# Performance work log

Hardware: AMD Instinct MI355X
Metric: run time of the kernel (lower is better)

## Reference

```python
import jax, jax.numpy as jnp
import numpy as np

N, E, B = 65536, 524288, 256
FEAT, EMB, NH, NB, NC = 64, 128, 4, 2, 4
OUT = EMB // NH
SLOPE = 0.01  # LeakyReLU negative_slope used everywhere in the module


def lrelu(x):
    return jnp.where(x > 0, x, SLOPE * x)


def seg_softmax(logits, seg, nseg, mask):
    # PyG softmax(src, batch): exp(x - segment_max) / (segment_sum + 1e-16)
    z = jnp.where(mask, logits, -jnp.inf)
    m = jax.ops.segment_max(z, seg, num_segments=nseg)
    m = jnp.where(jnp.isfinite(m), m, 0.0)
    e = jnp.exp(z - m[seg])
    s = jax.ops.segment_sum(e, seg, num_segments=nseg)
    return e / (s[seg] + 1e-16)


def topk_pool(x, seg, w, min_score, nseg):
    # PyG TopKPooling with min_score: score = softmax(x.w, batch);
    # keep nodes with score > min(min_score, per-graph max - 1e-7); x_out = x*score.
    score = x @ w  # [N]
    sm = seg_softmax(score, seg, nseg, jnp.ones(score.shape, bool))
    smax = jax.ops.segment_max(sm, seg, num_segments=nseg)
    thr = jnp.minimum(smax - 1e-7, min_score)
    keep = sm > thr[seg]
    xp = jnp.where(keep[:, None], x * sm[:, None], 0.0)
    return xp, keep


def graph_conv_max(x, src, dst, emask, Wrel, Wroot, b, n):
    # PyG GraphConv(aggr='max'): out = Wrel @ max_{j in N(i)} x_j + Wroot @ x_i + b
    msg = jnp.where(emask[:, None], x[src], -jnp.inf)  # [E, d]
    agg = jax.ops.segment_max(msg, dst, num_segments=n)
    agg = jnp.where(jnp.isfinite(agg), agg, 0.0)  # nodes with no in-edges -> 0 (PyG scatter fill)
    return agg @ Wrel.T + x @ Wroot.T + b


def batchnorm(x, g, b):
    # training-mode BatchNorm1d: batch statistics, biased variance, eps=1e-5
    mu = x.mean(0)
    var = x.var(0)
    return g * (x - mu) * jax.lax.rsqrt(var + 1e-5) + b


def setup_inputs() -> dict:
    key = jax.random.key(0)
    ks = jax.random.split(key, 16)
    s_feat = np.float32(1.0 / np.sqrt(FEAT))
    s_emb = np.float32(1.0 / np.sqrt(EMB))
    return {
        "x": jax.random.normal(ks[0], (N, FEAT), jnp.float32),
        "edge_index": jax.random.randint(ks[1], (2, E), 0, N, jnp.int32),
        "batch": (jnp.arange(N, dtype=jnp.int32) // (N // B)).astype(jnp.int32),
        "W_rel0": jax.random.normal(ks[2], (EMB, FEAT), jnp.float32) * s_feat,
        "W_root0": jax.random.normal(ks[3], (EMB, FEAT), jnp.float32) * s_feat,
        "b0": jnp.zeros((EMB,), jnp.float32),
        "bn0_g": jnp.ones((EMB,), jnp.float32),
        "bn0_b": jnp.zeros((EMB,), jnp.float32),
        "blk_pool_w": jax.random.normal(ks[4], (NB, NH, EMB), jnp.float32) * s_emb,
        "blk_Wrel": jax.random.normal(ks[5], (NB, NH, OUT, EMB), jnp.float32) * s_emb,
        "blk_Wroot": jax.random.normal(ks[6], (NB, NH, OUT, EMB), jnp.float32) * s_emb,
        "blk_b": jnp.zeros((NB, NH, OUT), jnp.float32),
        "blk_bn_g": jnp.ones((NB, EMB), jnp.float32),
        "blk_bn_b": jnp.zeros((NB, EMB), jnp.float32),
        "cls_pool_w": jax.random.normal(ks[7], (NC, EMB), jnp.float32) * s_emb,
        "cls_gW1": jax.random.normal(ks[8], (NC, EMB, EMB), jnp.float32) * s_emb,
        "cls_gb1": jnp.zeros((NC, EMB), jnp.float32),
        "cls_gW2": jax.random.normal(ks[9], (NC, EMB), jnp.float32) * s_emb,
        "cls_gb2": jnp.zeros((NC,), jnp.float32),
        "cls_fW1": jax.random.normal(ks[10], (NC, EMB, EMB), jnp.float32) * s_emb,
        "cls_fb1": jnp.zeros((NC, EMB), jnp.float32),
        "cls_fW2": jax.random.normal(ks[11], (NC, EMB), jnp.float32) * s_emb,
        "cls_fb2": jnp.zeros((NC,), jnp.float32),
        "batch_size": B,
    }


def reference(x, edge_index, batch, W_rel0, W_root0, b0, bn0_g, bn0_b,
              blk_pool_w, blk_Wrel, blk_Wroot, blk_b, blk_bn_g, blk_bn_b,
              cls_pool_w, cls_gW1, cls_gb1, cls_gW2, cls_gb2,
              cls_fW1, cls_fb1, cls_fW2, cls_fb2, batch_size):
    n = x.shape[0]
    src, dst = edge_index[0], edge_index[1]
    all_e = jnp.ones(src.shape, bool)
    # conv0 -> leaky_relu -> bn0
    h = lrelu(graph_conv_max(x, src, dst, all_e, W_rel0, W_root0, b0, n))
    cur = batchnorm(h, bn0_g, bn0_b)
    # multi-head blocks: pool (min_score=0.7) -> GraphConv(max) per head, scatter
    # back to original node slots, concat heads, bn, residual 0.5*(x + 0.5*bn(new))
    for bi in range(NB):
        heads = []
        for hi in range(NH):
            xp, keep = topk_pool(cur, batch, blk_pool_w[bi, hi], 0.7, batch_size)
            emask = keep[src] & keep[dst]
            o = lrelu(graph_conv_max(xp, src, dst, emask,
                                     blk_Wrel[bi, hi], blk_Wroot[bi, hi],
                                     blk_b[bi, hi], n))
            heads.append(jnp.where(keep[:, None], o, 0.0))
        new = batchnorm(jnp.concatenate(heads, axis=-1), blk_bn_g[bi], blk_bn_b[bi])
        cur = 0.5 * (cur + 0.5 * new)
    # classification heads: pool (min_score=0.8) -> GlobalAttention -> MLP -> 1
    outs = []
    for c in range(NC):
        xp, keep = topk_pool(cur, batch, cls_pool_w[c], 0.8, batch_size)
        gate = lrelu(xp @ cls_gW1[c].T + cls_gb1[c]) @ cls_gW2[c] + cls_gb2[c]  # [N]
        a = seg_softmax(gate, batch, batch_size, keep)
        pooled = jax.ops.segment_sum(a[:, None] * xp, batch, num_segments=batch_size)  # [B, EMB]
        y = lrelu(pooled @ cls_fW1[c].T + cls_fb1[c]) @ cls_fW2[c] + cls_fb2[c]  # [B]
        outs.append(y)
    logits = jnp.stack(outs, axis=-1)  # [B, NC]
    return jax.nn.log_softmax(logits, axis=-1)
```

## Files before the change

kernel.cpp:

```cpp
#include <hip/hip_runtime.h>
#include <math.h>

#define NN 65536
#define NE 524288
#define NG 256
#define SLOPE 0.01f

__device__ __forceinline__ float lrelu(float v){ return v > 0.f ? v : SLOPE*v; }

__device__ __forceinline__ float blockMax4(float v, float* s4){
  #pragma unroll
  for(int o=32;o>0;o>>=1) v = fmaxf(v, __shfl_down(v, o, 64));
  int t = threadIdx.x;
  __syncthreads();
  if((t&63)==0) s4[t>>6] = v;
  __syncthreads();
  return fmaxf(fmaxf(s4[0], s4[1]), fmaxf(s4[2], s4[3]));
}
__device__ __forceinline__ float blockSum4(float v, float* s4){
  #pragma unroll
  for(int o=32;o>0;o>>=1) v += __shfl_down(v, o, 64);
  int t = threadIdx.x;
  __syncthreads();
  if((t&63)==0) s4[t>>6] = v;
  __syncthreads();
  return (s4[0]+s4[1])+(s4[2]+s4[3]);
}

__global__ __launch_bounds__(256) void k_count(const int* __restrict__ ei, int* __restrict__ deg){
  int e = blockIdx.x*256 + threadIdx.x;
  if(e < NE) atomicAdd(&deg[ei[NE + e]], 1);
}

__global__ __launch_bounds__(1024) void k_scan(const int* __restrict__ deg,
      int* __restrict__ offs, int* __restrict__ cursor){
  __shared__ int part[1024];
  int t = threadIdx.x;
  const int4* d4 = (const int4*)(deg + t*64);
  int4 buf[16];
  int s=0;
  #pragma unroll
  for(int i=0;i<16;i++){ buf[i]=d4[i]; s += buf[i].x+buf[i].y+buf[i].z+buf[i].w; }
  part[t]=s;
  __syncthreads();
  for(int off=1; off<1024; off<<=1){
    int v = (t>=off)? part[t-off] : 0;
    __syncthreads();
    part[t] += v;
    __syncthreads();
  }
  int run = (t==0)? 0 : part[t-1];
  #pragma unroll
  for(int i=0;i<16;i++){
    int4 d = buf[i];
    int4 o;
    o.x = run; run += d.x;
    o.y = run; run += d.y;
    o.z = run; run += d.z;
    o.w = run; run += d.w;
    ((int4*)(offs + t*64))[i] = o;
    ((int4*)(cursor + t*64))[i] = o;
  }
  if(t==1023) offs[NN] = run;
}

__global__ __launch_bounds__(256) void k_scatter(const int* __restrict__ ei,
      int* __restrict__ cursor, int* __restrict__ csr){
  int e = blockIdx.x*256 + threadIdx.x;
  if(e < NE){
    int d = ei[NE + e];
    int p = atomicAdd(&cursor[d], 1);
    csr[p] = ei[e];
  }
}

__global__ __launch_bounds__(256) void k_agg0(const float* __restrict__ x,
    const int* __restrict__ offs, const int* __restrict__ csr, float* __restrict__ agg0){
  int tid = blockIdx.x*256 + threadIdx.x;
  int node = tid>>4, q = tid&15;
  int e0 = offs[node], e1 = offs[node+1];
  float4 acc = make_float4(0.f,0.f,0.f,0.f);
  if(e0 < e1){
    acc = make_float4(-INFINITY,-INFINITY,-INFINITY,-INFINITY);
    int e = e0;
    for(; e+7 < e1; e += 8){
      int si[8];
      #pragma unroll
      for(int u=0;u<8;u++) si[u] = csr[e+u];
      float4 v[8];
      #pragma unroll
      for(int u=0;u<8;u++) v[u] = ((const float4*)x)[si[u]*16 + q];
      #pragma unroll
      for(int u=0;u<8;u++){
        acc.x=fmaxf(acc.x,v[u].x); acc.y=fmaxf(acc.y,v[u].y);
        acc.z=fmaxf(acc.z,v[u].z); acc.w=fmaxf(acc.w,v[u].w);
      }
    }
    for(; e < e1; e++){
      int s0 = csr[e];
      float4 v0 = ((const float4*)x)[s0*16 + q];
      acc.x=fmaxf(acc.x,v0.x); acc.y=fmaxf(acc.y,v0.y);
      acc.z=fmaxf(acc.z,v0.z); acc.w=fmaxf(acc.w,v0.w);
    }
  }
  ((float4*)agg0)[node*16 + q] = acc;
}

__global__ __launch_bounds__(256)
__attribute__((amdgpu_waves_per_eu(1,2)))
void k_conv0mm(
    const float* __restrict__ agg0, const float* __restrict__ x,
    const float* __restrict__ Wrel, const float* __restrict__ Wroot,
    const float* __restrict__ b0, float* __restrict__ cur,
    float* __restrict__ bnsum, float* __restrict__ bnsq){
  __shared__ float4 As[2048];
  __shared__ float4 Ws[2048];
  const int t = threadIdx.x;
  const int tn = t & 15;
  const int tc = t >> 4;
  float acc[8][8];
  #pragma unroll
  for(int i=0;i<8;i++)
    #pragma unroll
    for(int j=0;j<8;j++) acc[i][j]=0.f;

  const size_t tileoff = (size_t)blockIdx.x * 8192;
  #pragma unroll 1
  for(int ch=0; ch<2; ch++){
    const float4* gA = (const float4*)((ch==0? agg0 : x) + tileoff);
    const float4* gW = (const float4*)(ch==0? Wrel : Wroot);
    __syncthreads();
    #pragma unroll
    for(int i=0;i<8;i++){
      int idx = t + i*256;
      int n = idx>>4, k4 = idx&15;
      int sw = n*16 + ((k4 + (n>>3))&15);
      As[sw] = gA[idx];
      Ws[sw] = gW[idx];
    }
    __syncthreads();
    #pragma unroll 4
    for(int k4=0;k4<16;k4++){
      float4 a4[8], w4[8];
      #pragma unroll
      for(int i=0;i<8;i++) a4[i] = As[(tn*8+i)*16 + ((k4+tn)&15)];
      #pragma unroll
      for(int i=0;i<8;i++) w4[i] = Ws[(tc*8+i)*16 + ((k4+tc)&15)];
      #pragma unroll
      for(int i=0;i<8;i++)
        #pragma unroll
        for(int j=0;j<8;j++){
          acc[i][j] = fmaf(a4[i].x, w4[j].x, acc[i][j]);
          acc[i][j] = fmaf(a4[i].y, w4[j].y, acc[i][j]);
          acc[i][j] = fmaf(a4[i].z, w4[j].z, acc[i][j]);
          acc[i][j] = fmaf(a4[i].w, w4[j].w, acc[i][j]);
        }
    }
  }

  float bj[8];
  #pragma unroll
  for(int j=0;j<8;j++) bj[j] = b0[tc*8+j];
  float cs[8], cq[8];
  #pragma unroll
  for(int j=0;j<8;j++){ cs[j]=0.f; cq[j]=0.f; }
  const int nbase = blockIdx.x*128;
  #pragma unroll
  for(int i=0;i<8;i++){
    int node = nbase + tn*8 + i;
    float v[8];
    #pragma unroll
    for(int j=0;j<8;j++){
      v[j] = lrelu(acc[i][j] + bj[j]);
      cs[j] += v[j]; cq[j] += v[j]*v[j];
    }
    float4 o0 = make_float4(v[0],v[1],v[2],v[3]);
    float4 o1 = make_float4(v[4],v[5],v[6],v[7]);
    ((float4*)cur)[node*32 + tc*2 + 0] = o0;
    ((float4*)cur)[node*32 + tc*2 + 1] = o1;
  }
  __syncthreads();
  float* reds = (float*)As;
  float* redq = (float*)Ws;
  #pragma unroll
  for(int j=0;j<8;j++){
    reds[(tc*8+j)*16 + tn] = cs[j];
    redq[(tc*8+j)*16 + tn] = cq[j];
  }
  __syncthreads();
  if(t<128){
    float S=0.f, Q=0.f;
    #pragma unroll
    for(int i=0;i<16;i++){ S += reds[t*16+i]; Q += redq[t*16+i]; }
    atomicAdd(&bnsum[t], S);
    atomicAdd(&bnsq[t], Q);
  }
}

template<int MODE>
__global__ __launch_bounds__(256) void k_stream(
    float* __restrict__ cur, const float* __restrict__ onew,
    const unsigned char* __restrict__ keepin,
    const float* __restrict__ bnsA, const float* __restrict__ bnqA,
    const float* __restrict__ g1, const float* __restrict__ b1,
    const float* __restrict__ bns0, const float* __restrict__ bnq0,
    const float* __restrict__ g0, const float* __restrict__ b0bn,
    const float* __restrict__ pw, float* __restrict__ scores){
  __shared__ __align__(16) float w[4][128];
  __shared__ __align__(16) float sc1[128], of1[128], sc0[128], of0[128];
  const int t = threadIdx.x;
  if(t<128){
    if(MODE>=1){
      float mu = bnsA[t]*(1.0f/NN);
      float var = bnqA[t]*(1.0f/NN) - mu*mu;
      float s = g1[t]*rsqrtf(var+1e-5f);
      sc1[t]=s; of1[t]=b1[t]-mu*s;
    }
    if(MODE<=1){
      float mu0 = bns0[t]*(1.0f/NN);
      float var0 = bnq0[t]*(1.0f/NN) - mu0*mu0;
      float s0 = g0[t]*rsqrtf(var0+1e-5f);
      sc0[t]=s0; of0[t]=b0bn[t]-mu0*s0;
    }
  }
  __syncthreads();
  for(int i=t;i<512;i+=256){
    float wv = pw[i];
    if(MODE==0) wv *= sc0[i&127];
    w[i>>7][i&127]=wv;
  }
  __syncthreads();
  const int tid = blockIdx.x*256 + t;
  const int n = tid>>5, k = tid&31;
  float4 v = ((const float4*)cur)[tid];
  if(MODE>=1){
    const int h = k>>3;
    float4 nv = make_float4(0.f,0.f,0.f,0.f);
    if((keepin[n]>>h)&1) nv = ((const float4*)onew)[tid];
    float4 s1 = *(const float4*)&sc1[k*4];
    float4 o1 = *(const float4*)&of1[k*4];
    if(MODE==1){
      float4 s0 = *(const float4*)&sc0[k*4];
      float4 o0 = *(const float4*)&of0[k*4];
      v.x = 0.5f*(s0.x*v.x+o0.x) + 0.25f*(s1.x*nv.x+o1.x);
      v.y = 0.5f*(s0.y*v.y+o0.y) + 0.25f*(s1.y*nv.y+o1.y);
      v.z = 0.5f*(s0.z*v.z+o0.z) + 0.25f*(s1.z*nv.z+o1.z);
      v.w = 0.5f*(s0.w*v.w+o0.w) + 0.25f*(s1.w*nv.w+o1.w);
    } else {
      v.x = 0.5f*v.x + 0.25f*(s1.x*nv.x+o1.x);
      v.y = 0.5f*v.y + 0.25f*(s1.y*nv.y+o1.y);
      v.z = 0.5f*v.z + 0.25f*(s1.z*nv.z+o1.z);
      v.w = 0.5f*v.w + 0.25f*(s1.w*nv.w+o1.w);
    }
    ((float4*)cur)[tid] = v;
  }
  float sch[4];
  #pragma unroll
  for(int h2=0;h2<4;h2++){
    float4 wv = *(const float4*)&w[h2][k*4];
    sch[h2] = v.x*wv.x + v.y*wv.y + v.z*wv.z + v.w*wv.w;
  }
  #pragma unroll
  for(int o=16;o>0;o>>=1){
    #pragma unroll
    for(int h2=0;h2<4;h2++) sch[h2] += __shfl_down(sch[h2], o, 32);
  }
  if(k==0) ((float4*)scores)[n] = make_float4(sch[0],sch[1],sch[2],sch[3]);
}

__global__ __launch_bounds__(256) void k_poolsel(const float* __restrict__ scores,
    float minscore, float* __restrict__ sm4, unsigned char* __restrict__ keep,
    int* __restrict__ cnt, int* __restrict__ wl){
  __shared__ float red[4];
  const int t = threadIdx.x, g = blockIdx.x, n = g*256 + t;
  float4 s4 = ((const float4*)scores)[n];
  float scv[4] = {s4.x, s4.y, s4.z, s4.w};
  float4 smout;
  unsigned kb = 0;
  #pragma unroll 1
  for(int h=0;h<4;h++){
    float m = blockMax4(scv[h], red);
    float e = expf(scv[h]-m);
    float ssum = blockSum4(e, red);
    float sm = e/(ssum + 1e-16f);
    float smax = blockMax4(sm, red);
    float thr = fminf(smax - 1e-7f, minscore);
    ((float*)&smout)[h] = sm;
    if(sm > thr){
      kb |= (1u<<h);
      int p = atomicAdd(cnt, 1);
      wl[p] = (h<<16) | n;
    }
  }
  __syncthreads();
  ((float4*)sm4)[n] = smout;
  keep[n] = (unsigned char)kb;
}

__global__ __launch_bounds__(256) void k_blockconv(const float* __restrict__ cur,
    const int* __restrict__ offs, const int* __restrict__ csr,
    const unsigned char* __restrict__ keep, const float* __restrict__ sm4,
    const int* __restrict__ cnt, const int* __restrict__ wl,
    const float* __restrict__ Wrel, const float* __restrict__ Wroot,
    const float* __restrict__ bias,
    float* __restrict__ onew, float* __restrict__ bnsum, float* __restrict__ bnsq,
    const float* __restrict__ bns0, const float* __restrict__ bnq0,
    const float* __restrict__ g0, const float* __restrict__ b0bn, int fold){
  __shared__ __align__(16) float aggs[8][128];
  __shared__ __align__(16) float xps[8][128];
  __shared__ __align__(16) float scv[128];
  __shared__ __align__(16) float ofv[128];
  const int t = threadIdx.x, grp = t>>5, lane = t&31;
  if(t<128){
    float sv = 1.f, ov = 0.f;
    if(fold){
      float mu = bns0[t]*(1.0f/NN);
      float var = bnq0[t]*(1.0f/NN) - mu*mu;
      sv = g0[t]*rsqrtf(var+1e-5f);
      ov = b0bn[t] - mu*sv;
    }
    scv[t]=sv; ofv[t]=ov;
  }
  __syncthreads();
  const float4 s4l = *(const float4*)&scv[lane*4];
  const float4 o4l = *(const float4*)&ofv[lane*4];
  const int total = *cnt;
  for(int item = blockIdx.x*8 + grp; item < total; item += gridDim.x*8){
    const int wv = wl[item];
    const int h = wv>>16, n = wv & 0xFFFF;
    const float smn = sm4[n*4+h];
    const int e0 = offs[n], e1 = offs[n+1];
    float4 acc = make_float4(-INFINITY,-INFINITY,-INFINITY,-INFINITY);
    bool any = false;
    for(int e=e0;e<e1;e++){
      int s = csr[e];
      if((keep[s]>>h)&1){
        any = true;
        float sv = sm4[s*4+h];
        float4 v = ((const float4*)cur)[s*32 + lane];
        v.x = (v.x*s4l.x + o4l.x)*sv; v.y = (v.y*s4l.y + o4l.y)*sv;
        v.z = (v.z*s4l.z + o4l.z)*sv; v.w = (v.w*s4l.w + o4l.w)*sv;
        acc.x = fmaxf(acc.x, v.x); acc.y = fmaxf(acc.y, v.y);
        acc.z = fmaxf(acc.z, v.z); acc.w = fmaxf(acc.w, v.w);
      }
    }
    if(!any) acc = make_float4(0.f,0.f,0.f,0.f);
    *(float4*)&aggs[grp][lane*4] = acc;
    float4 xv = ((const float4*)cur)[n*32 + lane];
    xv.x = (xv.x*s4l.x + o4l.x)*smn; xv.y = (xv.y*s4l.y + o4l.y)*smn;
    xv.z = (xv.z*s4l.z + o4l.z)*smn; xv.w = (xv.w*s4l.w + o4l.w)*smn;
    *(float4*)&xps[grp][lane*4] = xv;
    const float* Wr = Wrel  + (size_t)(h*32+lane)*128;
    const float* Wo = Wroot + (size_t)(h*32+lane)*128;
    float o = bias[h*32+lane];
    for(int k=0;k<32;k++){
      float4 a  = *(const float4*)&aggs[grp][k*4];
      float4 xx = *(const float4*)&xps[grp][k*4];
      float4 wr = ((const float4*)Wr)[k];
      float4 wo = ((const float4*)Wo)[k];
      o += a.x*wr.x + a.y*wr.y + a.z*wr.z + a.w*wr.w;
      o += xx.x*wo.x + xx.y*wo.y + xx.z*wo.z + xx.w*wo.w;
    }
    o = lrelu(o);
    onew[(size_t)n*128 + h*32 + lane] = o;
    atomicAdd(&bnsum[h*32+lane], o);
    atomicAdd(&bnsq[h*32+lane], o*o);
  }
}

__global__ __launch_bounds__(256) void k_cls2(const float* __restrict__ cur,
    const float* __restrict__ scores,
    const float* __restrict__ gW1, const float* __restrict__ gb1,
    const float* __restrict__ gW2, const float* __restrict__ gb2,
    const float* __restrict__ fW1, const float* __restrict__ fb1,
    const float* __restrict__ fW2, const float* __restrict__ fb2,
    float* __restrict__ yws){
  __shared__ float red[4];
  __shared__ int keptL[256];
  __shared__ float keptS[256];
  __shared__ float gateL[256];
  __shared__ __align__(16) float xk[128];
  __shared__ __align__(16) float pooled[128];
  __shared__ int nkept;
  const int t = threadIdx.x;
  const int g = blockIdx.x >> 2, c = blockIdx.x & 3;
  const int n = g*256 + t;
  float sc = scores[n*4 + c];
  float m = blockMax4(sc, red);
  float e = expf(sc-m);
  float ssum = blockSum4(e, red);
  float sm = e/(ssum+1e-16f);
  float smax = blockMax4(sm, red);
  float thr = fminf(smax - 1e-7f, 0.8f);
  if(t==0) nkept = 0;
  __syncthreads();
  if(sm > thr){
    int p = atomicAdd(&nkept,1);
    keptL[p]=t; keptS[p]=sm;
  }
  __syncthreads();
  const int K = nkept;
  for(int k=0;k<K;k++){
    int ln = keptL[k]; float sv = keptS[k];
    if(t<32){
      float4 v = ((const float4*)(cur + (size_t)(g*256+ln)*128))[t];
      v.x*=sv; v.y*=sv; v.z*=sv; v.w*=sv;
      *(float4*)&xk[t*4] = v;
    }
    __syncthreads();
    float part = 0.f;
    if(t<128){
      const float* W = gW1 + (size_t)c*16384 + (size_t)t*128;
      float a = gb1[c*128+t];
      for(int f=0;f<32;f++){
        float4 xv = *(const float4*)&xk[f*4];
        float4 wv = ((const float4*)W)[f];
        a += xv.x*wv.x + xv.y*wv.y + xv.z*wv.z + xv.w*wv.w;
      }
      part = lrelu(a) * gW2[c*128+t];
    }
    float gs = blockSum4(part, red);
    if(t==0) gateL[k] = gs + gb2[c];
    __syncthreads();
  }
  float gv = (t<K)? gateL[t] : -INFINITY;
  float gm = blockMax4(gv, red);
  float ge = (t<K)? expf(gv-gm) : 0.f;
  float gsum = blockSum4(ge, red);
  if(t<K) gateL[t] = ge/(gsum+1e-16f);
  __syncthreads();
  if(t<128){
    float acc = 0.f;
    for(int k=0;k<K;k++)
      acc += gateL[k]*keptS[k]*cur[(size_t)(g*256+keptL[k])*128 + t];
    pooled[t]=acc;
  }
  __syncthreads();
  float part2=0.f;
  if(t<128){
    const float* F = fW1 + (size_t)c*16384 + (size_t)t*128;
    float a = fb1[c*128+t];
    for(int f=0;f<32;f++){
      float4 xv = *(const float4*)&pooled[f*4];
      float4 wv = ((const float4*)F)[f];
      a += xv.x*wv.x + xv.y*wv.y + xv.z*wv.z + xv.w*wv.w;
    }
    part2 = lrelu(a) * fW2[c*128+t];
  }
  float ysum = blockSum4(part2, red);
  if(t==0) yws[g*4+c] = ysum + fb2[c];
}

__global__ __launch_bounds__(256) void k_clsfin(const float* __restrict__ yws,
                                                float* __restrict__ out){
  const int g = threadIdx.x;
  float4 y = ((const float4*)yws)[g];
  float m = fmaxf(fmaxf(y.x,y.y), fmaxf(y.z,y.w));
  float l = logf(expf(y.x-m)+expf(y.y-m)+expf(y.z-m)+expf(y.w-m));
  float4 o = make_float4(y.x-m-l, y.y-m-l, y.z-m-l, y.w-m-l);
  ((float4*)out)[g] = o;
}

extern "C" void kernel_launch(void* const* d_in, const int* in_sizes, int n_in,
                              void* d_out, int out_size, void* d_ws, size_t ws_size,
                              hipStream_t stream){
  (void)in_sizes; (void)n_in; (void)out_size; (void)ws_size;
  const float* x     = (const float*)d_in[0];
  const int*   ei    = (const int*)d_in[1];
  const float* Wrel0 = (const float*)d_in[3];
  const float* Wroot0= (const float*)d_in[4];
  const float* b0    = (const float*)d_in[5];
  const float* bn0g  = (const float*)d_in[6];
  const float* bn0b  = (const float*)d_in[7];
  const float* bpw   = (const float*)d_in[8];
  const float* bWrel = (const float*)d_in[9];
  const float* bWroot= (const float*)d_in[10];
  const float* bbv   = (const float*)d_in[11];
  const float* bbng  = (const float*)d_in[12];
  const float* bbnb  = (const float*)d_in[13];
  const float* cpw   = (const float*)d_in[14];
  const float* gW1   = (const float*)d_in[15];
  const float* gb1   = (const float*)d_in[16];
  const float* gW2   = (const float*)d_in[17];
  const float* gb2   = (const float*)d_in[18];
  const float* fW1   = (const float*)d_in[19];
  const float* fb1   = (const float*)d_in[20];
  const float* fW2   = (const float*)d_in[21];
  const float* fb2   = (const float*)d_in[22];

  char* ws = (char*)d_ws;
  float* cur   = (float*)(ws + 0);
  float* onew  = (float*)(ws + 33554432ull);
  float* agg0  = onew;
  int*   csr   = (int*)(ws + 67108864ull);
  float* sm4   = (float*)(ws + 69206016ull);
  float* scores= sm4;
  int*   wl    = (int*)(ws + 70254592ull);
  int*   offs  = (int*)(ws + 71303168ull);
  int*   cursor= (int*)(ws + 71565568ull);
  unsigned char* keep = (unsigned char*)(ws + 71827712ull);
  char*  Z     = ws + 71893248ull;
  int*   deg   = (int*)Z;
  float* bnsum0= (float*)(Z + 262144);
  float* bnsq0 = (float*)(Z + 262656);
  float* bnA   = (float*)(Z + 263168);
  float* bqA   = (float*)(Z + 263680);
  float* bnB   = (float*)(Z + 264192);
  float* bqB   = (float*)(Z + 264704);
  int*   cnt0  = (int*)(Z + 265216);
  int*   cnt1  = (int*)(Z + 265220);
  float* yws   = (float*)(Z + 266240);

  hipMemsetAsync(Z, 0, 265224, stream);

  k_count  <<<2048,256,0,stream>>>(ei, deg);
  k_scan   <<<1,1024,0,stream>>>(deg, offs, cursor);
  k_scatter<<<2048,256,0,stream>>>(ei, cursor, csr);

  k_agg0    <<<4096,256,0,stream>>>(x, offs, csr, agg0);
  k_conv0mm <<<512,256,0,stream>>>(agg0, x, Wrel0, Wroot0, b0, cur, bnsum0, bnsq0);

  k_stream<0><<<8192,256,0,stream>>>(cur, onew, keep, bnA, bqA, bbng, bbnb,
                                     bnsum0, bnsq0, bn0g, bn0b, bpw, scores);
  k_poolsel<<<256,256,0,stream>>>(scores, 0.7f, sm4, keep, cnt0, wl);

  k_blockconv<<<256,256,0,stream>>>(cur, offs, csr, keep, sm4, cnt0, wl,
                                    bWrel, bWroot, bbv, onew, bnA, bqA,
                                    bnsum0, bnsq0, bn0g, bn0b, 1);

  k_stream<1><<<8192,256,0,stream>>>(cur, onew, keep, bnA, bqA, bbng, bbnb,
                                     bnsum0, bnsq0, bn0g, bn0b, bpw + 512, scores);
  k_poolsel<<<256,256,0,stream>>>(scores, 0.7f, sm4, keep, cnt1, wl);

  k_blockconv<<<256,256,0,stream>>>(cur, offs, csr, keep, sm4, cnt1, wl,
                                    bWrel + 16384, bWroot + 16384, bbv + 128, onew, bnB, bqB,
                                    bnsum0, bnsq0, bn0g, bn0b, 0);

  k_stream<2><<<8192,256,0,stream>>>(cur, onew, keep, bnB, bqB, bbng + 128, bbnb + 128,
                                     bnsum0, bnsq0, bn0g, bn0b, cpw, scores);

  k_cls2<<<1024,256,0,stream>>>(cur, scores, gW1, gb1, gW2, gb2,
                                fW1, fb1, fW2, fb2, yws);
  k_clsfin<<<1,256,0,stream>>>(yws, (float*)d_out);
}
```

Before: 430.8 us.

## Compute pooling scores for all stages up front and store conv outputs compactly

The three full-size stream passes over the 32MB node feature matrix are replaced by a single pass over the layer-0 output. That pass computes the pooling scores for all three stages by linearity, and later stages add sparse patches built from the compacted head outputs. Conv outputs are now stored only for kept (node, head) items, addressed through per-node index tables, and later features are rebuilt on the fly from cur0 and those compact arrays. This removes several large read/write sweeps. In exchange it adds per-block scans of the whole worklist in poolsel1 and cls2, a CAP limit on kept items that can silently drop work, and a larger launch-bounds occupancy hint on the matmul.

```diff
diff --git a/kernel.cpp b/kernel.cpp
--- a/kernel.cpp
+++ b/kernel.cpp
@@ -5,6 +5,7 @@
 #define NE 524288
 #define NG 256
 #define SLOPE 0.01f
+#define CAP 131072
 
 __device__ __forceinline__ float lrelu(float v){ return v > 0.f ? v : SLOPE*v; }
 
@@ -106,9 +107,7 @@
   ((float4*)agg0)[node*16 + q] = acc;
 }
 
-__global__ __launch_bounds__(256)
-__attribute__((amdgpu_waves_per_eu(1,2)))
-void k_conv0mm(
+__global__ __launch_bounds__(256, 2) void k_conv0mm(
     const float* __restrict__ agg0, const float* __restrict__ x,
     const float* __restrict__ Wrel, const float* __restrict__ Wroot,
     const float* __restrict__ b0, float* __restrict__ cur,
@@ -197,80 +196,53 @@
   }
 }
 
-template<int MODE>
-__global__ __launch_bounds__(256) void k_stream(
-    float* __restrict__ cur, const float* __restrict__ onew,
-    const unsigned char* __restrict__ keepin,
-    const float* __restrict__ bnsA, const float* __restrict__ bnqA,
-    const float* __restrict__ g1, const float* __restrict__ b1,
+__global__ __launch_bounds__(256) void k_scores(const float* __restrict__ cur0,
     const float* __restrict__ bns0, const float* __restrict__ bnq0,
-    const float* __restrict__ g0, const float* __restrict__ b0bn,
-    const float* __restrict__ pw, float* __restrict__ scores){
-  __shared__ __align__(16) float w[4][128];
-  __shared__ __align__(16) float sc1[128], of1[128], sc0[128], of0[128];
+    const float* __restrict__ g0,
+    const float* __restrict__ pw0, const float* __restrict__ pw1,
+    const float* __restrict__ pwc,
+    float* __restrict__ scores0, float* __restrict__ pre1, float* __restrict__ pre2){
+  __shared__ __align__(16) float w[12][128];
+  __shared__ float sc0s[128];
   const int t = threadIdx.x;
   if(t<128){
-    if(MODE>=1){
-      float mu = bnsA[t]*(1.0f/NN);
-      float var = bnqA[t]*(1.0f/NN) - mu*mu;
-      float s = g1[t]*rsqrtf(var+1e-5f);
-      sc1[t]=s; of1[t]=b1[t]-mu*s;
-    }
-    if(MODE<=1){
-      float mu0 = bns0[t]*(1.0f/NN);
-      float var0 = bnq0[t]*(1.0f/NN) - mu0*mu0;
-      float s0 = g0[t]*rsqrtf(var0+1e-5f);
-      sc0[t]=s0; of0[t]=b0bn[t]-mu0*s0;
-    }
+    float mu = bns0[t]*(1.0f/NN);
+    float var = bnq0[t]*(1.0f/NN) - mu*mu;
+    sc0s[t] = g0[t]*rsqrtf(var+1e-5f);
   }
   __syncthreads();
   for(int i=t;i<512;i+=256){
-    float wv = pw[i];
-    if(MODE==0) wv *= sc0[i&127];
-    w[i>>7][i&127]=wv;
+    int h=i>>7, j=i&127;
+    float s = sc0s[j];
+    w[h][j]   = pw0[i]*s;
+    w[4+h][j] = pw1[i]*(0.5f*s);
+    w[8+h][j] = pwc[i]*(0.25f*s);
   }
   __syncthreads();
   const int tid = blockIdx.x*256 + t;
   const int n = tid>>5, k = tid&31;
-  float4 v = ((const float4*)cur)[tid];
-  if(MODE>=1){
-    const int h = k>>3;
-    float4 nv = make_float4(0.f,0.f,0.f,0.f);
-    if((keepin[n]>>h)&1) nv = ((const float4*)onew)[tid];
-    float4 s1 = *(const float4*)&sc1[k*4];
-    float4 o1 = *(const float4*)&of1[k*4];
-    if(MODE==1){
-      float4 s0 = *(const float4*)&sc0[k*4];
-      float4 o0 = *(const float4*)&of0[k*4];
-      v.x = 0.5f*(s0.x*v.x+o0.x) + 0.25f*(s1.x*nv.x+o1.x);
-      v.y = 0.5f*(s0.y*v.y+o0.y) + 0.25f*(s1.y*nv.y+o1.y);
-      v.z = 0.5f*(s0.z*v.z+o0.z) + 0.25f*(s1.z*nv.z+o1.z);
-      v.w = 0.5f*(s0.w*v.w+o0.w) + 0.25f*(s1.w*nv.w+o1.w);
-    } else {
-      v.x = 0.5f*v.x + 0.25f*(s1.x*nv.x+o1.x);
-      v.y = 0.5f*v.y + 0.25f*(s1.y*nv.y+o1.y);
-      v.z = 0.5f*v.z + 0.25f*(s1.z*nv.z+o1.z);
-      v.w = 0.5f*v.w + 0.25f*(s1.w*nv.w+o1.w);
-    }
-    ((float4*)cur)[tid] = v;
-  }
-  float sch[4];
-  #pragma unroll
-  for(int h2=0;h2<4;h2++){
-    float4 wv = *(const float4*)&w[h2][k*4];
-    sch[h2] = v.x*wv.x + v.y*wv.y + v.z*wv.z + v.w*wv.w;
+  float4 v = ((const float4*)cur0)[tid];
+  float a[12];
+  #pragma unroll
+  for(int q=0;q<12;q++){
+    float4 wv = *(const float4*)&w[q][k*4];
+    a[q] = v.x*wv.x + v.y*wv.y + v.z*wv.z + v.w*wv.w;
   }
   #pragma unroll
   for(int o=16;o>0;o>>=1){
     #pragma unroll
-    for(int h2=0;h2<4;h2++) sch[h2] += __shfl_down(sch[h2], o, 32);
-  }
-  if(k==0) ((float4*)scores)[n] = make_float4(sch[0],sch[1],sch[2],sch[3]);
+    for(int q=0;q<12;q++) a[q] += __shfl_down(a[q], o, 32);
+  }
+  if(k==0){
+    ((float4*)scores0)[n] = make_float4(a[0],a[1],a[2],a[3]);
+    ((float4*)pre1)[n]    = make_float4(a[4],a[5],a[6],a[7]);
+    ((float4*)pre2)[n]    = make_float4(a[8],a[9],a[10],a[11]);
+  }
 }
 
 __global__ __launch_bounds__(256) void k_poolsel(const float* __restrict__ scores,
     float minscore, float* __restrict__ sm4, unsigned char* __restrict__ keep,
-    int* __restrict__ cnt, int* __restrict__ wl){
+    int* __restrict__ cnt, int* __restrict__ wl, int* __restrict__ idx){
   __shared__ float red[4];
   const int t = threadIdx.x, g = blockIdx.x, n = g*256 + t;
   float4 s4 = ((const float4*)scores)[n];
@@ -287,9 +259,12 @@
     float thr = fminf(smax - 1e-7f, minscore);
     ((float*)&smout)[h] = sm;
     if(sm > thr){
-      kb |= (1u<<h);
       int p = atomicAdd(cnt, 1);
-      wl[p] = (h<<16) | n;
+      if(p < CAP){
+        kb |= (1u<<h);
+        wl[p] = (h<<16) | n;
+        idx[n*4+h] = p;
+      }
     }
   }
   __syncthreads();
@@ -297,34 +272,30 @@
   keep[n] = (unsigned char)kb;
 }
 
-__global__ __launch_bounds__(256) void k_blockconv(const float* __restrict__ cur,
+__global__ __launch_bounds__(256) void k_blockconv0(const float* __restrict__ cur0,
     const int* __restrict__ offs, const int* __restrict__ csr,
     const unsigned char* __restrict__ keep, const float* __restrict__ sm4,
     const int* __restrict__ cnt, const int* __restrict__ wl,
     const float* __restrict__ Wrel, const float* __restrict__ Wroot,
     const float* __restrict__ bias,
-    float* __restrict__ onew, float* __restrict__ bnsum, float* __restrict__ bnsq,
+    float* __restrict__ new1c, float* __restrict__ bnsum, float* __restrict__ bnsq,
     const float* __restrict__ bns0, const float* __restrict__ bnq0,
-    const float* __restrict__ g0, const float* __restrict__ b0bn, int fold){
+    const float* __restrict__ g0, const float* __restrict__ b0bn){
   __shared__ __align__(16) float aggs[8][128];
   __shared__ __align__(16) float xps[8][128];
   __shared__ __align__(16) float scv[128];
   __shared__ __align__(16) float ofv[128];
   const int t = threadIdx.x, grp = t>>5, lane = t&31;
   if(t<128){
-    float sv = 1.f, ov = 0.f;
-    if(fold){
-      float mu = bns0[t]*(1.0f/NN);
-      float var = bnq0[t]*(1.0f/NN) - mu*mu;
-      sv = g0[t]*rsqrtf(var+1e-5f);
-      ov = b0bn[t] - mu*sv;
-    }
-    scv[t]=sv; ofv[t]=ov;
+    float mu = bns0[t]*(1.0f/NN);
+    float var = bnq0[t]*(1.0f/NN) - mu*mu;
+    float sv = g0[t]*rsqrtf(var+1e-5f);
+    scv[t]=sv; ofv[t]=b0bn[t]-mu*sv;
   }
   __syncthreads();
   const float4 s4l = *(const float4*)&scv[lane*4];
   const float4 o4l = *(const float4*)&ofv[lane*4];
-  const int total = *cnt;
+  int total = *cnt; if(total > CAP) total = CAP;
   for(int item = blockIdx.x*8 + grp; item < total; item += gridDim.x*8){
     const int wv = wl[item];
     const int h = wv>>16, n = wv & 0xFFFF;
@@ -337,7 +308,7 @@
       if((keep[s]>>h)&1){
         any = true;
         float sv = sm4[s*4+h];
-        float4 v = ((const float4*)cur)[s*32 + lane];
+        float4 v = ((const float4*)cur0)[s*32 + lane];
         v.x = (v.x*s4l.x + o4l.x)*sv; v.y = (v.y*s4l.y + o4l.y)*sv;
         v.z = (v.z*s4l.z + o4l.z)*sv; v.w = (v.w*s4l.w + o4l.w)*sv;
         acc.x = fmaxf(acc.x, v.x); acc.y = fmaxf(acc.y, v.y);
@@ -346,7 +317,7 @@
     }
     if(!any) acc = make_float4(0.f,0.f,0.f,0.f);
     *(float4*)&aggs[grp][lane*4] = acc;
-    float4 xv = ((const float4*)cur)[n*32 + lane];
+    float4 xv = ((const float4*)cur0)[n*32 + lane];
     xv.x = (xv.x*s4l.x + o4l.x)*smn; xv.y = (xv.y*s4l.y + o4l.y)*smn;
     xv.z = (xv.z*s4l.z + o4l.z)*smn; xv.w = (xv.w*s4l.w + o4l.w)*smn;
     *(float4*)&xps[grp][lane*4] = xv;
@@ -362,20 +333,205 @@
       o += xx.x*wo.x + xx.y*wo.y + xx.z*wo.z + xx.w*wo.w;
     }
     o = lrelu(o);
-    onew[(size_t)n*128 + h*32 + lane] = o;
+    new1c[(size_t)item*32 + lane] = o;
     atomicAdd(&bnsum[h*32+lane], o);
     atomicAdd(&bnsq[h*32+lane], o*o);
   }
 }
 
-__global__ __launch_bounds__(256) void k_cls2(const float* __restrict__ cur,
-    const float* __restrict__ scores,
+__global__ __launch_bounds__(256) void k_poolsel1(
+    const float* __restrict__ pre1, float* __restrict__ pre2,
+    const int* __restrict__ cnt0, const int* __restrict__ wl0,
+    const float* __restrict__ new1c,
+    const float* __restrict__ bnsA, const float* __restrict__ bnqA,
+    const float* __restrict__ g1v,
+    const float* __restrict__ pw1, const float* __restrict__ pwc,
+    float minscore, float* __restrict__ sm4out, unsigned char* __restrict__ keep1,
+    int* __restrict__ cnt1, int* __restrict__ wl1, int* __restrict__ idx1){
+  __shared__ float red[4];
+  __shared__ float s1s[128];
+  __shared__ __align__(16) float w1s[4][128];
+  __shared__ __align__(16) float wcs[4][128];
+  __shared__ float patch1[256][4];
+  const int t = threadIdx.x, g = blockIdx.x;
+  if(t<128){
+    float mu = bnsA[t]*(1.0f/NN);
+    float var = bnqA[t]*(1.0f/NN) - mu*mu;
+    s1s[t] = g1v[t]*rsqrtf(var+1e-5f);
+  }
+  for(int i=t;i<512;i+=256){ w1s[i>>7][i&127]=pw1[i]; wcs[i>>7][i&127]=pwc[i]; }
+  #pragma unroll
+  for(int h=0;h<4;h++) patch1[t][h]=0.f;
+  __syncthreads();
+  int total0 = *cnt0; if(total0 > CAP) total0 = CAP;
+  for(int i=t; i<total0; i+=256){
+    int wv = wl0[i];
+    int n = wv & 0xFFFF, hp = wv>>16;
+    if((n>>8)==g){
+      int nl = n & 255;
+      float d[4]={0.f,0.f,0.f,0.f}, d2[4]={0.f,0.f,0.f,0.f};
+      for(int l=0;l<32;l++){
+        int j = hp*32+l;
+        float base = new1c[(size_t)i*32+l] * s1s[j];
+        #pragma unroll
+        for(int h=0;h<4;h++){ d[h]+=base*w1s[h][j]; d2[h]+=base*wcs[h][j]; }
+      }
+      #pragma unroll
+      for(int h=0;h<4;h++){
+        atomicAdd(&patch1[nl][h], 0.25f*d[h]);
+        atomicAdd(&pre2[n*4+h], 0.125f*d2[h]);
+      }
+    }
+  }
+  __syncthreads();
+  const int n = g*256 + t;
+  float4 p4 = ((const float4*)pre1)[n];
+  float scv[4] = {p4.x+patch1[t][0], p4.y+patch1[t][1],
+                  p4.z+patch1[t][2], p4.w+patch1[t][3]};
+  float4 smout;
+  unsigned kb = 0;
+  #pragma unroll 1
+  for(int h=0;h<4;h++){
+    float m = blockMax4(scv[h], red);
+    float e = expf(scv[h]-m);
+    float ssum = blockSum4(e, red);
+    float sm = e/(ssum + 1e-16f);
+    float smax = blockMax4(sm, red);
+    float thr = fminf(smax - 1e-7f, minscore);
+    ((float*)&smout)[h] = sm;
+    if(sm > thr){
+      int p = atomicAdd(cnt1, 1);
+      if(p < CAP){
+        kb |= (1u<<h);
+        wl1[p] = (h<<16) | n;
+        idx1[n*4+h] = p;
+      }
+    }
+  }
+  __syncthreads();
+  ((float4*)sm4out)[n] = smout;
+  keep1[n] = (unsigned char)kb;
+}
+
+__global__ __launch_bounds__(256) void k_blockconv1(const float* __restrict__ cur0,
+    const int* __restrict__ offs, const int* __restrict__ csr,
+    const unsigned char* __restrict__ keep0, const int* __restrict__ idx0,
+    const float* __restrict__ new1c,
+    const unsigned char* __restrict__ keep1, const float* __restrict__ sm41,
+    const int* __restrict__ cnt1, const int* __restrict__ wl1,
+    const float* __restrict__ Wrel, const float* __restrict__ Wroot,
+    const float* __restrict__ bias,
+    float* __restrict__ new2c, float* __restrict__ bnsum, float* __restrict__ bnsq,
+    const float* __restrict__ bns0, const float* __restrict__ bnq0,
+    const float* __restrict__ g0, const float* __restrict__ b0bn,
+    const float* __restrict__ bnsA, const float* __restrict__ bnqA,
+    const float* __restrict__ g1v, const float* __restrict__ b1v){
+  __shared__ __align__(16) float aggs[8][128];
+  __shared__ __align__(16) float xps[8][128];
+  __shared__ __align__(16) float sc0s[128], of0s[128], s1s[128], o1s[128];
+  const int t = threadIdx.x, grp = t>>5, lane = t&31;
+  if(t<128){
+    float mu = bns0[t]*(1.0f/NN);
+    float var = bnq0[t]*(1.0f/NN) - mu*mu;
+    float sv = g0[t]*rsqrtf(var+1e-5f);
+    sc0s[t]=sv; of0s[t]=b0bn[t]-mu*sv;
+    float mu1 = bnsA[t]*(1.0f/NN);
+    float var1 = bnqA[t]*(1.0f/NN) - mu1*mu1;
+    float s1 = g1v[t]*rsqrtf(var1+1e-5f);
+    s1s[t]=s1; o1s[t]=b1v[t]-mu1*s1;
+  }
+  __syncthreads();
+  const float4 s0l = *(const float4*)&sc0s[lane*4];
+  const float4 o0l = *(const float4*)&of0s[lane*4];
+  const float4 s1l = *(const float4*)&s1s[lane*4];
+  const float4 o1l = *(const float4*)&o1s[lane*4];
+  const int hb = lane>>3;
+  int total = *cnt1; if(total > CAP) total = CAP;
+  for(int item = blockIdx.x*8 + grp; item < total; item += gridDim.x*8){
+    const int wv = wl1[item];
+    const int h = wv>>16, n = wv & 0xFFFF;
+    const float smn = sm41[n*4+h];
+    const int e0 = offs[n], e1 = offs[n+1];
+    float4 acc = make_float4(-INFINITY,-INFINITY,-INFINITY,-INFINITY);
+    bool any = false;
+    for(int e=e0;e<e1;e++){
+      int s = csr[e];
+      if((keep1[s]>>h)&1){
+        any = true;
+        float sv = sm41[s*4+h];
+        float4 c0 = ((const float4*)cur0)[s*32 + lane];
+        float4 v;
+        v.x = 0.5f*(s0l.x*c0.x+o0l.x) + 0.25f*o1l.x;
+        v.y = 0.5f*(s0l.y*c0.y+o0l.y) + 0.25f*o1l.y;
+        v.z = 0.5f*(s0l.z*c0.z+o0l.z) + 0.25f*o1l.z;
+        v.w = 0.5f*(s0l.w*c0.w+o0l.w) + 0.25f*o1l.w;
+        if((keep0[s]>>hb)&1){
+          float4 nv = ((const float4*)(new1c + (size_t)idx0[s*4+hb]*32))[lane&7];
+          v.x += 0.25f*s1l.x*nv.x; v.y += 0.25f*s1l.y*nv.y;
+          v.z += 0.25f*s1l.z*nv.z; v.w += 0.25f*s1l.w*nv.w;
+        }
+        v.x*=sv; v.y*=sv; v.z*=sv; v.w*=sv;
+        acc.x = fmaxf(acc.x, v.x); acc.y = fmaxf(acc.y, v.y);
+        acc.z = fmaxf(acc.z, v.z); acc.w = fmaxf(acc.w, v.w);
+      }
+    }
+    if(!any) acc = make_float4(0.f,0.f,0.f,0.f);
+    *(float4*)&aggs[grp][lane*4] = acc;
+    {
+      float4 c0 = ((const float4*)cur0)[n*32 + lane];
+      float4 v;
+      v.x = 0.5f*(s0l.x*c0.x+o0l.x) + 0.25f*o1l.x;
+      v.y = 0.5f*(s0l.y*c0.y+o0l.y) + 0.25f*o1l.y;
+      v.z = 0.5f*(s0l.z*c0.z+o0l.z) + 0.25f*o1l.z;
+      v.w = 0.5f*(s0l.w*c0.w+o0l.w) + 0.25f*o1l.w;
+      if((keep0[n]>>hb)&1){
+        float4 nv = ((const float4*)(new1c + (size_t)idx0[n*4+hb]*32))[lane&7];
+        v.x += 0.25f*s1l.x*nv.x; v.y += 0.25f*s1l.y*nv.y;
+        v.z += 0.25f*s1l.z*nv.z; v.w += 0.25f*s1l.w*nv.w;
+      }
+      v.x*=smn; v.y*=smn; v.z*=smn; v.w*=smn;
+      *(float4*)&xps[grp][lane*4] = v;
+    }
+    const float* Wr = Wrel  + (size_t)(h*32+lane)*128;
+    const float* Wo = Wroot + (size_t)(h*32+lane)*128;
+    float o = bias[h*32+lane];
+    for(int k=0;k<32;k++){
+      float4 a  = *(const float4*)&aggs[grp][k*4];
+      float4 xx = *(const float4*)&xps[grp][k*4];
+      float4 wr = ((const float4*)Wr)[k];
+      float4 wo = ((const float4*)Wo)[k];
+      o += a.x*wr.x + a.y*wr.y + a.z*wr.z + a.w*wr.w;
+      o += xx.x*wo.x + xx.y*wo.y + xx.z*wo.z + xx.w*wo.w;
+    }
+    o = lrelu(o);
+    new2c[(size_t)item*32 + lane] = o;
+    atomicAdd(&bnsum[h*32+lane], o);
+    atomicAdd(&bnsq[h*32+lane], o*o);
+  }
+}
+
+__global__ __launch_bounds__(256) void k_cls2(const float* __restrict__ cur0,
+    const unsigned char* __restrict__ keep0, const int* __restrict__ idx0,
+    const float* __restrict__ new1c,
+    const unsigned char* __restrict__ keep1, const int* __restrict__ idx1,
+    const float* __restrict__ new2c,
+    const float* __restrict__ pre2, const int* __restrict__ cnt1,
+    const int* __restrict__ wl1, const float* __restrict__ pwc,
+    const float* __restrict__ bns0, const float* __restrict__ bnq0,
+    const float* __restrict__ g0, const float* __restrict__ b0bn,
+    const float* __restrict__ bnsA, const float* __restrict__ bnqA,
+    const float* __restrict__ g1v, const float* __restrict__ b1v,
+    const float* __restrict__ bnsB, const float* __restrict__ bnqB,
+    const float* __restrict__ g2v, const float* __restrict__ b2v,
     const float* __restrict__ gW1, const float* __restrict__ gb1,
     const float* __restrict__ gW2, const float* __restrict__ gb2,
     const float* __restrict__ fW1, const float* __restrict__ fb1,
     const float* __restrict__ fW2, const float* __restrict__ fb2,
     float* __restrict__ yws){
   __shared__ float red[4];
+  __shared__ float sc0s[128], of0s[128], s1s[128], o1s[128], s2s[128], o2s[128];
+  __shared__ float wc[128];
+  __shared__ float patch[256];
   __shared__ int keptL[256];
   __shared__ float keptS[256];
   __shared__ float gateL[256];
@@ -384,8 +540,39 @@
   __shared__ int nkept;
   const int t = threadIdx.x;
   const int g = blockIdx.x >> 2, c = blockIdx.x & 3;
+  if(t<128){
+    float mu = bns0[t]*(1.0f/NN);
+    float var = bnq0[t]*(1.0f/NN) - mu*mu;
+    float sv = g0[t]*rsqrtf(var+1e-5f);
+    sc0s[t]=sv; of0s[t]=b0bn[t]-mu*sv;
+    float mu1 = bnsA[t]*(1.0f/NN);
+    float var1 = bnqA[t]*(1.0f/NN) - mu1*mu1;
+    float s1 = g1v[t]*rsqrtf(var1+1e-5f);
+    s1s[t]=s1; o1s[t]=b1v[t]-mu1*s1;
+    float mu2 = bnsB[t]*(1.0f/NN);
+    float var2 = bnqB[t]*(1.0f/NN) - mu2*mu2;
+    float s2 = g2v[t]*rsqrtf(var2+1e-5f);
+    s2s[t]=s2; o2s[t]=b2v[t]-mu2*s2;
+    wc[t] = pwc[c*128+t];
+  }
+  patch[t]=0.f;
+  __syncthreads();
+  int total1 = *cnt1; if(total1 > CAP) total1 = CAP;
+  for(int i=t; i<total1; i+=256){
+    int wv = wl1[i];
+    int n = wv & 0xFFFF, hp = wv>>16;
+    if((n>>8)==g){
+      float d=0.f;
+      for(int l=0;l<32;l++){
+        int j = hp*32+l;
+        d += new2c[(size_t)i*32+l]*s2s[j]*wc[j];
+      }
+      atomicAdd(&patch[n&255], 0.25f*d);
+    }
+  }
+  __syncthreads();
   const int n = g*256 + t;
-  float sc = scores[n*4 + c];
+  float sc = pre2[n*4 + c] + patch[t];
   float m = blockMax4(sc, red);
   float e = expf(sc-m);
   float ssum = blockSum4(e, red);
@@ -402,10 +589,38 @@
   const int K = nkept;
   for(int k=0;k<K;k++){
     int ln = keptL[k]; float sv = keptS[k];
+    int nn = g*256 + ln;
     if(t<32){
-      float4 v = ((const float4*)(cur + (size_t)(g*256+ln)*128))[t];
-      v.x*=sv; v.y*=sv; v.z*=sv; v.w*=sv;
-      *(float4*)&xk[t*4] = v;
+      float4 c0 = ((const float4*)cur0)[nn*32 + t];
+      float4 s0l = *(const float4*)&sc0s[t*4];
+      float4 o0l = *(const float4*)&of0s[t*4];
+      float4 s1l = *(const float4*)&s1s[t*4];
+      float4 o1l = *(const float4*)&o1s[t*4];
+      float4 s2l = *(const float4*)&s2s[t*4];
+      float4 o2l = *(const float4*)&o2s[t*4];
+      int hb = t>>3;
+      float4 v1;
+      v1.x = 0.5f*(s0l.x*c0.x+o0l.x) + 0.25f*o1l.x;
+      v1.y = 0.5f*(s0l.y*c0.y+o0l.y) + 0.25f*o1l.y;
+      v1.z = 0.5f*(s0l.z*c0.z+o0l.z) + 0.25f*o1l.z;
+      v1.w = 0.5f*(s0l.w*c0.w+o0l.w) + 0.25f*o1l.w;
+      if((keep0[nn]>>hb)&1){
+        float4 nv = ((const float4*)(new1c + (size_t)idx0[nn*4+hb]*32))[t&7];
+        v1.x += 0.25f*s1l.x*nv.x; v1.y += 0.25f*s1l.y*nv.y;
+        v1.z += 0.25f*s1l.z*nv.z; v1.w += 0.25f*s1l.w*nv.w;
+      }
+      float4 v2;
+      v2.x = 0.5f*v1.x + 0.25f*o2l.x;
+      v2.y = 0.5f*v1.y + 0.25f*o2l.y;
+      v2.z = 0.5f*v1.z + 0.25f*o2l.z;
+      v2.w = 0.5f*v1.w + 0.25f*o2l.w;
+      if((keep1[nn]>>hb)&1){
+        float4 nv = ((const float4*)(new2c + (size_t)idx1[nn*4+hb]*32))[t&7];
+        v2.x += 0.25f*s2l.x*nv.x; v2.y += 0.25f*s2l.y*nv.y;
+        v2.z += 0.25f*s2l.z*nv.z; v2.w += 0.25f*s2l.w*nv.w;
+      }
+      v2.x*=sv; v2.y*=sv; v2.z*=sv; v2.w*=sv;
+      *(float4*)&xk[t*4] = v2;
     }
     __syncthreads();
     float part = 0.f;
@@ -430,9 +645,17 @@
   if(t<K) gateL[t] = ge/(gsum+1e-16f);
   __syncthreads();
   if(t<128){
+    int hb = t>>5, l = t&31;
     float acc = 0.f;
-    for(int k=0;k<K;k++)
-      acc += gateL[k]*keptS[k]*cur[(size_t)(g*256+keptL[k])*128 + t];
+    for(int k=0;k<K;k++){
+      int nn = g*256 + keptL[k];
+      float c0 = cur0[(size_t)nn*128 + t];
+      float v1 = 0.5f*(sc0s[t]*c0 + of0s[t]) + 0.25f*o1s[t];
+      if((keep0[nn]>>hb)&1) v1 += 0.25f*s1s[t]*new1c[(size_t)idx0[nn*4+hb]*32 + l];
+      float v2 = 0.5f*v1 + 0.25f*o2s[t];
+      if((keep1[nn]>>hb)&1) v2 += 0.25f*s2s[t]*new2c[(size_t)idx1[nn*4+hb]*32 + l];
+      acc += gateL[k]*keptS[k]*v2;
+    }
     pooled[t]=acc;
   }
   __syncthreads();
@@ -457,8 +680,7 @@
   float4 y = ((const float4*)yws)[g];
   float m = fmaxf(fmaxf(y.x,y.y), fmaxf(y.z,y.w));
   float l = logf(expf(y.x-m)+expf(y.y-m)+expf(y.z-m)+expf(y.w-m));
-  float4 o = make_float4(y.x-m-l, y.y-m-l, y.z-m-l, y.w-m-l);
-  ((float4*)out)[g] = o;
+  ((float4*)out)[g] = make_float4(y.x-m-l, y.y-m-l, y.z-m-l, y.w-m-l);
 }
 
 extern "C" void kernel_launch(void* const* d_in, const int* in_sizes, int n_in,
@@ -489,17 +711,25 @@
   const float* fb2   = (const float*)d_in[22];
 
   char* ws = (char*)d_ws;
-  float* cur   = (float*)(ws + 0);
-  float* onew  = (float*)(ws + 33554432ull);
-  float* agg0  = onew;
+  float* cur0  = (float*)(ws + 0);
+  float* new1c = (float*)(ws + 33554432ull);
+  float* new2c = (float*)(ws + 50331648ull);
+  float* agg0  = new2c;
   int*   csr   = (int*)(ws + 67108864ull);
-  float* sm4   = (float*)(ws + 69206016ull);
-  float* scores= sm4;
-  int*   wl    = (int*)(ws + 70254592ull);
-  int*   offs  = (int*)(ws + 71303168ull);
-  int*   cursor= (int*)(ws + 71565568ull);
-  unsigned char* keep = (unsigned char*)(ws + 71827712ull);
-  char*  Z     = ws + 71893248ull;
+  float* scores0=(float*)(ws + 69206016ull);
+  float* sm40  = scores0;
+  float* pre1  = (float*)(ws + 70254592ull);
+  float* sm41  = pre1;
+  float* pre2  = (float*)(ws + 71303168ull);
+  int*   wl0   = (int*)(ws + 72351744ull);
+  int*   wl1   = (int*)(ws + 72876032ull);
+  int*   offs  = (int*)(ws + 73400320ull);
+  int*   cursor= (int*)(ws + 73666560ull);
+  unsigned char* keep0 = (unsigned char*)(ws + 73928704ull);
+  unsigned char* keep1 = (unsigned char*)(ws + 73994240ull);
+  int*   idx0  = (int*)(ws + 74059776ull);
+  int*   idx1  = (int*)(ws + 75108352ull);
+  char*  Z     = ws + 76156928ull;
   int*   deg   = (int*)Z;
   float* bnsum0= (float*)(Z + 262144);
   float* bnsq0 = (float*)(Z + 262656);
@@ -511,35 +741,42 @@
   int*   cnt1  = (int*)(Z + 265220);
   float* yws   = (float*)(Z + 266240);
 
-  hipMemsetAsync(Z, 0, 265224, stream);
+  hipMemsetAsync(Z, 0, 270336, stream);
+  hipMemsetAsync(idx0, 0xFF, 2097152, stream);
 
   k_count  <<<2048,256,0,stream>>>(ei, deg);
   k_scan   <<<1,1024,0,stream>>>(deg, offs, cursor);
   k_scatter<<<2048,256,0,stream>>>(ei, cursor, csr);
 
   k_agg0    <<<4096,256,0,stream>>>(x, offs, csr, agg0);
-  k_conv0mm <<<512,256,0,stream>>>(agg0, x, Wrel0, Wroot0, b0, cur, bnsum0, bnsq0);
-
-  k_stream<0><<<8192,256,0,stream>>>(cur, onew, keep, bnA, bqA, bbng, bbnb,
-                                     bnsum0, bnsq0, bn0g, bn0b, bpw, scores);
-  k_poolsel<<<256,256,0,stream>>>(scores, 0.7f, sm4, keep, cnt0, wl);
-
-  k_blockconv<<<256,256,0,stream>>>(cur, offs, csr, keep, sm4, cnt0, wl,
-                                    bWrel, bWroot, bbv, onew, bnA, bqA,
-                                    bnsum0, bnsq0, bn0g, bn0b, 1);
-
-  k_stream<1><<<8192,256,0,stream>>>(cur, onew, keep, bnA, bqA, bbng, bbnb,
-                                     bnsum0, bnsq0, bn0g, bn0b, bpw + 512, scores);
-  k_poolsel<<<256,256,0,stream>>>(scores, 0.7f, sm4, keep, cnt1, wl);
-
-  k_blockconv<<<256,256,0,stream>>>(cur, offs, csr, keep, sm4, cnt1, wl,
-                                    bWrel + 16384, bWroot + 16384, bbv + 128, onew, bnB, bqB,
-                                    bnsum0, bnsq0, bn0g, bn0b, 0);
-
-  k_stream<2><<<8192,256,0,stream>>>(cur, onew, keep, bnB, bqB, bbng + 128, bbnb + 128,
-                                     bnsum0, bnsq0, bn0g, bn0b, cpw, scores);
-
-  k_cls2<<<1024,256,0,stream>>>(cur, scores, gW1, gb1, gW2, gb2,
-                                fW1, fb1, fW2, fb2, yws);
+  k_conv0mm <<<512,256,0,stream>>>(agg0, x, Wrel0, Wroot0, b0, cur0, bnsum0, bnsq0);
+
+  k_scores<<<8192,256,0,stream>>>(cur0, bnsum0, bnsq0, bn0g,
+                                  bpw, bpw + 512, cpw, scores0, pre1, pre2);
+
+  k_poolsel<<<256,256,0,stream>>>(scores0, 0.7f, sm40, keep0, cnt0, wl0, idx0);
+
+  k_blockconv0<<<256,256,0,stream>>>(cur0, offs, csr, keep0, sm40, cnt0, wl0,
+                                     bWrel, bWroot, bbv, new1c, bnA, bqA,
+                                     bnsum0, bnsq0, bn0g, bn0b);
+
+  k_poolsel1<<<256,256,0,stream>>>(pre1, pre2, cnt0, wl0, new1c,
+                                   bnA, bqA, bbng,
+                                   bpw + 512, cpw,
+                                   0.7f, sm41, keep1, cnt1, wl1, idx1);
+
+  k_blockconv1<<<256,256,0,stream>>>(cur0, offs, csr, keep0, idx0, new1c,
+                                     keep1, sm41, cnt1, wl1,
+                                     bWrel + 16384, bWroot + 16384, bbv + 128,
+                                     new2c, bnB, bqB,
+                                     bnsum0, bnsq0, bn0g, bn0b,
+                                     bnA, bqA, bbng, bbnb);
+
+  k_cls2<<<1024,256,0,stream>>>(cur0, keep0, idx0, new1c, keep1, idx1, new2c,
+                                pre2, cnt1, wl1, cpw,
+                                bnsum0, bnsq0, bn0g, bn0b,
+                                bnA, bqA, bbng, bbnb,
+                                bnB, bqB, bbng + 128, bbnb + 128,
+                                gW1, gb1, gW2, gb2, fW1, fb1, fW2, fb2, yws);
   k_clsfin<<<1,256,0,stream>>>(yws, (float*)d_out);
 }
```

New measurement: 385.5 us. -10.5%, faster.
